# Optimization experiments

Hardware: AMD Instinct MI355X
Metric: run time of the kernel (lower is better)

Reference implementation:

```python
import jax, jax.numpy as jnp
import numpy as np

B, L, D = 4, 2048, 1024


def setup_inputs() -> dict:
    key = jax.random.key(0)
    ks = jax.random.split(key, 7)
    scale = 1.0 / np.sqrt(D)
    x = jax.random.normal(ks[0], (B, L, D), dtype=jnp.float32)
    wq = jax.random.normal(ks[1], (D, D), dtype=jnp.float32) * scale
    wk = jax.random.normal(ks[2], (D, D), dtype=jnp.float32) * scale
    wv = jax.random.normal(ks[3], (D, D), dtype=jnp.float32) * scale
    bq = jnp.zeros((D,), dtype=jnp.float32)
    bk = jnp.zeros((D,), dtype=jnp.float32)
    bv = jnp.zeros((D,), dtype=jnp.float32)
    # causal decoder mask, shape [B, 1, L, L] as produced by nn.make_causal_mask
    causal = jnp.tril(jnp.ones((L, L), dtype=bool))
    mask = jnp.broadcast_to(causal[None, None, :, :], (B, 1, L, L))
    return {"x": x, "mask": mask, "wq": wq, "bq": bq, "wk": wk, "bk": bk, "wv": wv, "bv": bv}


def reference(x, mask, wq, bq, wk, bk, wv, bv):
    # q/k/v projections (Dense with bias)
    q = x @ wq + bq            # [B, L, D]
    k = x @ wk + bk
    v = x @ wv + bv
    depth = q.shape[-1]
    q = q / jnp.sqrt(jnp.asarray(depth, dtype=q.dtype))
    attn = jnp.einsum('bqd,bkd->bqk', q, k)          # [B, L, L]
    attn = jnp.where(jnp.squeeze(mask), attn, -999999)
    attn = jax.nn.softmax(attn, axis=-1)
    out = attn @ v                                    # [B, L, D]
    return out
```

## Files before the change

### kernel.cpp

```cpp
#include <hip/hip_runtime.h>

typedef __bf16 bf16_t;
typedef __attribute__((ext_vector_type(8))) __bf16 bf16x8;
typedef __attribute__((ext_vector_type(4))) __bf16 bf16x4;
typedef __attribute__((ext_vector_type(4))) float f32x4;

#define B_  4
#define L_  2048
#define D_  1024
#define M_  (B_*L_)
#define N3_ (3*D_)

__device__ __forceinline__ void gload_lds16(const void* g, void* l) {
  __builtin_amdgcn_global_load_lds(
      (__attribute__((address_space(1))) void*)(g),
      (__attribute__((address_space(3))) void*)(l), 16, 0, 0);
}

__device__ __forceinline__ void stage_half(const bf16_t* __restrict__ g, int ld, int grow0,
                                           int k0, bf16_t* lds_tile, int h, int tid) {
  const int lane = tid & 63;
  const int csrc = ((lane & 7) ^ (lane >> 3)) << 3;
  const int rsub = tid >> 3;
  bf16_t* l0 = lds_tile + (size_t)(h * 128 + ((tid >> 6) << 3)) * 64;
  const bf16_t* g0 = g + (size_t)(grow0 + h * 128 + rsub) * ld + (k0 + csrc);
  gload_lds16(g0, l0);
  gload_lds16(g0 + (size_t)64 * ld, l0 + 64 * 64);
}

#define KTILE(J, AC, AN1, AN2, BCr, BNx, bC, bN)                                  \
  do {                                                                            \
    const int j_ = (J);                                                           \
    _Pragma("unroll")                                                             \
    for (int mi = 0; mi < 4; ++mi) {                                              \
      aM1_[mi][0] = *(const bf16x8*)(AC + abase + (4 + mi) * 2048 + co0);         \
      aM1_[mi][1] = *(const bf16x8*)(AC + abase + (4 + mi) * 2048 + co1);         \
    }                                                                             \
    if (j_ + 2 < NT) {                                                            \
      stage_half(A, lda, r0, (j_ + 2) * 64, AN2, 0, tid);                         \
      stage_half(A, lda, r0, (j_ + 2) * 64, AN2, 1, tid);                         \
    }                                                                             \
    asm volatile("s_waitcnt lgkmcnt(8)" ::: "memory");                            \
    __builtin_amdgcn_sched_barrier(0);                                            \
    __builtin_amdgcn_s_setprio(1);                                                \
    _Pragma("unroll")                                                             \
    for (int mi = 0; mi < 4; ++mi)                                                \
      _Pragma("unroll")                                                           \
      for (int ni = 0; ni < 2; ++ni) {                                            \
        acc[mi][ni] = __builtin_amdgcn_mfma_f32_16x16x32_bf16(                    \
            bC[ni][0], aM0_[mi][0], acc[mi][ni], 0, 0, 0);                        \
        acc[mi][ni] = __builtin_amdgcn_mfma_f32_16x16x32_bf16(                    \
            bC[ni][1], aM0_[mi][1], acc[mi][ni], 0, 0, 0);                        \
      }                                                                           \
    __builtin_amdgcn_s_setprio(0);                                                \
    if (j_ + 2 < NT) asm volatile("s_waitcnt vmcnt(4)" ::: "memory");             \
    else             asm volatile("s_waitcnt vmcnt(0)" ::: "memory");             \
    asm volatile("s_barrier" ::: "memory");                                       \
    if (j_ + 1 < NT) {                                                            \
      _Pragma("unroll")                                                           \
      for (int mi = 0; mi < 4; ++mi) {                                            \
        aM0_[mi][0] = *(const bf16x8*)(AN1 + abase + mi * 2048 + co0);            \
        aM0_[mi][1] = *(const bf16x8*)(AN1 + abase + mi * 2048 + co1);            \
      }                                                                           \
      _Pragma("unroll")                                                           \
      for (int ni = 0; ni < 2; ++ni) {                                            \
        bN[ni][0] = *(const bf16x8*)(BNx + bbase + ni * 1024 + co0);              \
        bN[ni][1] = *(const bf16x8*)(BNx + bbase + ni * 1024 + co1);              \
      }                                                                           \
      if (j_ + 2 < NT)                                                            \
        stage_half(Bt, ldb, c0, (j_ + 2) * 64, BCr, 0, tid);                      \
      asm volatile("s_waitcnt lgkmcnt(12)" ::: "memory");                         \
    } else {                                                                      \
      asm volatile("s_waitcnt lgkmcnt(0)" ::: "memory");                          \
    }                                                                             \
    __builtin_amdgcn_sched_barrier(0);                                            \
    __builtin_amdgcn_s_setprio(1);                                                \
    _Pragma("unroll")                                                             \
    for (int mi = 0; mi < 4; ++mi)                                                \
      _Pragma("unroll")                                                           \
      for (int ni = 0; ni < 2; ++ni) {                                            \
        acc[4 + mi][ni] = __builtin_amdgcn_mfma_f32_16x16x32_bf16(                \
            bC[ni][0], aM1_[mi][0], acc[4 + mi][ni], 0, 0, 0);                    \
        acc[4 + mi][ni] = __builtin_amdgcn_mfma_f32_16x16x32_bf16(                \
            bC[ni][1], aM1_[mi][1], acc[4 + mi][ni], 0, 0, 0);                    \
      }                                                                           \
    __builtin_amdgcn_s_setprio(0);                                                \
    asm volatile("s_barrier" ::: "memory");                                       \
  } while (0)

template<bool OUT_BF16, bool CAUSAL, bool VARK, bool PROJ>
__global__ __launch_bounds__(512, 2)
void gemm8(const bf16_t* __restrict__ A, int lda, long sA,
           const bf16_t* __restrict__ Bt, int ldb, long sB,
           void* __restrict__ Cv, int ldc, long sC,
           const float* __restrict__ b0, const float* __restrict__ b1,
           const float* __restrict__ b2, int K)
{
  const int gx = gridDim.x;
  const int nwg = gx * gridDim.y;
  const int orig = blockIdx.y * gx + blockIdx.x;
  const int swz = (orig & 7) * (nwg >> 3) + (orig >> 3);
  const int bx = swz % gx, by = swz / gx;
  if (CAUSAL && bx > 2 * by + 1) return;

  const int z = blockIdx.z;
  A  += (size_t)z * sA;
  Bt += (size_t)z * sB;

  const int r0 = by * 256, c0 = bx * 128;
  const int kend = VARK ? min(K, r0 + 256) : K;
  const int NT = kend >> 6;

  extern __shared__ __align__(16) bf16_t smem[];
  bf16_t* Ab0 = smem;
  bf16_t* Ab1 = smem + 16384;
  bf16_t* Ab2 = smem + 32768;
  bf16_t* Bb0 = smem + 49152;
  bf16_t* Bb1 = smem + 57344;

  const int tid = threadIdx.x;
  const int wid = tid >> 6, lane = tid & 63;
  const int wm = wid >> 2, wn = wid & 3;
  const int rl = lane & 15, cg = lane >> 4, x0 = lane & 7;
  const int co0 = ((cg ^ x0) << 3);
  const int co1 = (((4 + cg) ^ x0) << 3);
  const int abase = (wm * 16 + rl) * 64;
  const int bbase = (wn * 32 + rl) * 64;

  f32x4 acc[8][2] = {};
  bf16x8 aM0_[4][2], aM1_[4][2];
  bf16x8 bA_[2][2], bB_[2][2];

  stage_half(A,  lda, r0, 0,  Ab0, 0, tid);
  stage_half(A,  lda, r0, 0,  Ab0, 1, tid);
  stage_half(Bt, ldb, c0, 0,  Bb0, 0, tid);
  stage_half(A,  lda, r0, 64, Ab1, 0, tid);
  stage_half(A,  lda, r0, 64, Ab1, 1, tid);
  stage_half(Bt, ldb, c0, 64, Bb1, 0, tid);
  asm volatile("s_waitcnt vmcnt(6)" ::: "memory");
  asm volatile("s_barrier" ::: "memory");
  #pragma unroll
  for (int mi = 0; mi < 4; ++mi) {
    aM0_[mi][0] = *(const bf16x8*)(Ab0 + abase + mi * 2048 + co0);
    aM0_[mi][1] = *(const bf16x8*)(Ab0 + abase + mi * 2048 + co1);
  }
  #pragma unroll
  for (int ni = 0; ni < 2; ++ni) {
    bA_[ni][0] = *(const bf16x8*)(Bb0 + bbase + ni * 1024 + co0);
    bA_[ni][1] = *(const bf16x8*)(Bb0 + bbase + ni * 1024 + co1);
  }

  bf16_t *A0 = Ab0, *A1 = Ab1, *A2 = Ab2;
  for (int j = 0; j < NT; j += 2) {
    KTILE(j,     A0, A1, A2, Bb0, Bb1, bA_, bB_);
    KTILE(j + 1, A1, A2, A0, Bb1, Bb0, bB_, bA_);
    bf16_t* t = A2; A2 = A1; A1 = A0; A0 = t;
  }

  const int ml = lane & 15, ng = cg * 4;
  #pragma unroll
  for (int mi = 0; mi < 8; ++mi) {
    const int r = r0 + mi * 32 + wm * 16 + ml;
    #pragma unroll
    for (int ni = 0; ni < 2; ++ni) {
      const int c = c0 + wn * 32 + ni * 16 + ng;
      f32x4 v = acc[mi][ni];
      if (PROJ) {
        const float* bias = (c < D_) ? b0 : (c < 2 * D_) ? b1 : b2;
        const float4 bb = *(const float4*)(bias + (c & (D_ - 1)));
        const float sc = (c < D_) ? 0.03125f : 1.0f;
        v[0] = (v[0] + bb.x) * sc; v[1] = (v[1] + bb.y) * sc;
        v[2] = (v[2] + bb.z) * sc; v[3] = (v[3] + bb.w) * sc;
      }
      if (OUT_BF16) {
        bf16x4 o = {(bf16_t)v[0], (bf16_t)v[1], (bf16_t)v[2], (bf16_t)v[3]};
        *(bf16x4*)((bf16_t*)Cv + (size_t)z * sC + (size_t)r * ldc + c) = o;
      } else {
        *(f32x4*)((float*)Cv + (size_t)z * sC + (size_t)r * ldc + c) = v;
      }
    }
  }
}

__device__ __forceinline__ float blk_red_max(float v, float* red, int lane, int wid) {
  #pragma unroll
  for (int o = 32; o; o >>= 1) v = fmaxf(v, __shfl_down(v, o));
  __syncthreads();
  if (lane == 0) red[wid] = v;
  __syncthreads();
  return fmaxf(fmaxf(red[0], red[1]), fmaxf(red[2], red[3]));
}
__device__ __forceinline__ float blk_red_sum(float v, float* red, int lane, int wid) {
  #pragma unroll
  for (int o = 32; o; o >>= 1) v += __shfl_down(v, o);
  __syncthreads();
  if (lane == 0) red[wid] = v;
  __syncthreads();
  return red[0] + red[1] + red[2] + red[3];
}

__global__ __launch_bounds__(256)
void softmax_causal(const bf16_t* __restrict__ S, bf16_t* __restrict__ P) {
  const int r = blockIdx.x;
  const int n = r + 1;
  const int kend = min(((n + 255) >> 8) << 8, L_);
  const bf16_t* row = S + (size_t)blockIdx.y * L_ * L_ + (size_t)r * L_;
  bf16_t* prow = P + (size_t)blockIdx.y * L_ * L_ + (size_t)r * L_;
  const int tid = threadIdx.x, lane = tid & 63, wid = tid >> 6;
  const int c0 = tid * 8;
  __shared__ float red[4];

  const bf16x8 v8 = *(const bf16x8*)(row + c0);
  float s[8];
  #pragma unroll
  for (int i = 0; i < 8; ++i)
    s[i] = (c0 + i < n) ? (float)v8[i] : -3.402823466e38f;

  float mx = s[0];
  #pragma unroll
  for (int i = 1; i < 8; ++i) mx = fmaxf(mx, s[i]);
  mx = blk_red_max(mx, red, lane, wid);

  float e[8]; float sum = 0.f;
  #pragma unroll
  for (int i = 0; i < 8; ++i) {
    const float v = (c0 + i < n) ? __expf(s[i] - mx) : 0.f;
    e[i] = v; sum += v;
  }
  sum = blk_red_sum(sum, red, lane, wid);
  const float inv = 1.0f / sum;

  if (c0 < kend) {
    bf16x8 o;
    #pragma unroll
    for (int i = 0; i < 8; ++i) o[i] = (bf16_t)(e[i] * inv);
    *(bf16x8*)(prow + c0) = o;
  }
}

__global__ void cvt_f32_bf16(const float* __restrict__ in, bf16_t* __restrict__ out, int n4) {
  const int stride = gridDim.x * blockDim.x;
  for (int i = blockIdx.x * blockDim.x + threadIdx.x; i < n4; i += stride) {
    const float4 v = ((const float4*)in)[i];
    bf16x4 o = { (bf16_t)v.x, (bf16_t)v.y, (bf16_t)v.z, (bf16_t)v.w };
    ((bf16x4*)out)[i] = o;
  }
}

__global__ void transpose_w3(const float* __restrict__ w0, const float* __restrict__ w1,
                             const float* __restrict__ w2, bf16_t* __restrict__ oT) {
  const float* w = blockIdx.z == 0 ? w0 : (blockIdx.z == 1 ? w1 : w2);
  bf16_t* o = oT + (size_t)blockIdx.z * D_ * D_;
  __shared__ float t[32][33];
  const int tx = threadIdx.x, ty = threadIdx.y;
  const int x  = blockIdx.x * 32 + tx;
  const int y0 = blockIdx.y * 32;
  #pragma unroll
  for (int j = 0; j < 4; ++j)
    t[ty + j * 8][tx] = w[(size_t)(y0 + ty + j * 8) * D_ + x];
  __syncthreads();
  const int x2 = y0 + tx;
  const int y2 = blockIdx.x * 32;
  #pragma unroll
  for (int j = 0; j < 4; ++j)
    o[(size_t)(y2 + ty + j * 8) * D_ + x2] = (bf16_t)t[tx][ty + j * 8];
}

__global__ void transpose_bf16(const bf16_t* __restrict__ in, int ld_in, int coff,
                               bf16_t* __restrict__ out, int R, int C) {
  __shared__ bf16_t t[32][34];
  const int tx = threadIdx.x, ty = threadIdx.y;
  const int x  = blockIdx.x * 32 + tx;
  const int y0 = blockIdx.y * 32;
  #pragma unroll
  for (int j = 0; j < 4; ++j)
    t[ty + j * 8][tx] = in[(size_t)(y0 + ty + j * 8) * ld_in + coff + x];
  __syncthreads();
  const int x2 = y0 + tx;
  const int y2 = blockIdx.x * 32;
  #pragma unroll
  for (int j = 0; j < 4; ++j)
    out[(size_t)(y2 + ty + j * 8) * R + x2] = t[tx][ty + j * 8];
}

extern "C" void kernel_launch(void* const* d_in, const int* in_sizes, int n_in,
                              void* d_out, int out_size, void* d_ws, size_t ws_size,
                              hipStream_t stream) {
  const float* x  = (const float*)d_in[0];
  const float* wq = (const float*)d_in[2];
  const float* bq = (const float*)d_in[3];
  const float* wk = (const float*)d_in[4];
  const float* bk = (const float*)d_in[5];
  const float* wv = (const float*)d_in[6];
  const float* bv = (const float*)d_in[7];
  float* out = (float*)d_out;

  bf16_t* xb   = (bf16_t*)d_ws;
  bf16_t* wT   = xb  + (size_t)M_ * D_;
  bf16_t* qkv  = wT  + (size_t)N3_ * D_;
  bf16_t* vbT  = qkv + (size_t)M_ * N3_;
  bf16_t* Sb   = vbT + (size_t)M_ * D_;
  bf16_t* Pfull = qkv;

  const size_t SMEM = 131072;

  cvt_f32_bf16<<<1024, 256, 0, stream>>>(x, xb, M_ * D_ / 4);
  transpose_w3<<<dim3(32, 32, 3), dim3(32, 8), 0, stream>>>(wq, wk, wv, wT);

  gemm8<true, false, false, true><<<dim3(N3_ / 128, M_ / 256), 512, SMEM, stream>>>(
      xb, D_, 0, wT, D_, 0, qkv, N3_, 0, bq, bk, bv, D_);

  transpose_bf16<<<dim3(D_ / 32, M_ / 32), dim3(32, 8), 0, stream>>>(qkv, N3_, 2 * D_, vbT, M_, D_);

  gemm8<true, true, false, false><<<dim3(L_ / 128, L_ / 256, B_), 512, SMEM, stream>>>(
      qkv, N3_, (long)L_ * N3_, qkv + D_, N3_, (long)L_ * N3_, Sb, L_, (long)L_ * L_,
      nullptr, nullptr, nullptr, D_);

  softmax_causal<<<dim3(L_, B_), 256, 0, stream>>>(Sb, Pfull);

  gemm8<false, false, true, false><<<dim3(D_ / 128, L_ / 256, B_), 512, SMEM, stream>>>(
      Pfull, L_, (long)L_ * L_, vbT, M_, (long)L_, out, D_, (long)L_ * D_,
      nullptr, nullptr, nullptr, L_);
}
```

Before: 179.2 us.

## Load-balance causal PV GEMM with split-K band jobs and partial-sum reduction

Replaces the uniform PV GEMM launch with a job kernel that assigns causal row bands to workgroups in balanced pairs. The longest bands are split along K, with one part written to a float workspace and then added back by a small reduction kernel. The aim is to remove the load imbalance caused by the triangular attention matrix, at the cost of an extra kernel launch and a read-modify-write of part of the output.

```diff
diff --git a/kernel.cpp b/kernel.cpp
--- a/kernel.cpp
+++ b/kernel.cpp
@@ -182,6 +182,116 @@
   }
 }
 
+__global__ __launch_bounds__(512, 2)
+void pv_job(const bf16_t* __restrict__ A_, int lda, long sA,
+            const bf16_t* __restrict__ Bt_, int ldb, long sB,
+            float* __restrict__ out, int ldc, long sC,
+            float* __restrict__ part)
+{
+  const int gx = gridDim.x;
+  const int nwg = gx * gridDim.y;
+  const int orig = blockIdx.y * gx + blockIdx.x;
+  const int swz = (orig & 7) * (nwg >> 3) + (orig >> 3);
+  const int bx = swz % gx, yy = swz / gx;
+
+  const int z = blockIdx.z;
+  const bf16_t* A  = A_  + (size_t)z * sA;
+  const bf16_t* Bt = Bt_ + (size_t)z * sB;
+  const int c0 = bx * 128;
+
+  int nseg = 1, band0, j00 = 0, nt0, band1 = 0, j01 = 0, nt1 = 0;
+  bool topart = false;
+  switch (yy) {
+    case 0:  band0 = 3; nt0 = 16; break;
+    case 1:  band0 = 4; nt0 = 20; break;
+    case 2:  nseg = 2; band0 = 0; nt0 = 4;  band1 = 7; j01 = 0; nt1 = 14; break;
+    case 3:  band0 = 7; j00 = 14; nt0 = 32; topart = true; break;
+    case 4:  nseg = 2; band0 = 1; nt0 = 8;  band1 = 6; j01 = 0; nt1 = 10; break;
+    case 5:  band0 = 6; j00 = 10; nt0 = 28; topart = true; break;
+    case 6:  nseg = 2; band0 = 2; nt0 = 12; band1 = 5; j01 = 0; nt1 = 6; break;
+    default: band0 = 5; j00 = 6;  nt0 = 24; topart = true; break;
+  }
+
+  extern __shared__ __align__(16) bf16_t smem[];
+  bf16_t* Ab0 = smem;
+  bf16_t* Ab1 = smem + 16384;
+  bf16_t* Ab2 = smem + 32768;
+  bf16_t* Bb0 = smem + 49152;
+  bf16_t* Bb1 = smem + 57344;
+
+  const int tid = threadIdx.x;
+  const int wid = tid >> 6, lane = tid & 63;
+  const int wm = wid >> 2, wn = wid & 3;
+  const int rl = lane & 15, cg = lane >> 4, x0 = lane & 7;
+  const int co0 = ((cg ^ x0) << 3);
+  const int co1 = (((4 + cg) ^ x0) << 3);
+  const int abase = (wm * 16 + rl) * 64;
+  const int bbase = (wn * 32 + rl) * 64;
+
+  for (int seg = 0; seg < nseg; ++seg) {
+    const int r0 = (seg ? band1 : band0) * 256;
+    const int j0 = seg ? j01 : j00;
+    const int NT = seg ? nt1 : nt0;
+    const bool pw = (seg == 0) && topart;
+
+    f32x4 acc[8][2] = {};
+    bf16x8 aM0_[4][2], aM1_[4][2];
+    bf16x8 bA_[2][2], bB_[2][2];
+
+    stage_half(A,  lda, r0, j0 * 64,       Ab0, 0, tid);
+    stage_half(A,  lda, r0, j0 * 64,       Ab0, 1, tid);
+    stage_half(Bt, ldb, c0, j0 * 64,       Bb0, 0, tid);
+    stage_half(A,  lda, r0, (j0 + 1) * 64, Ab1, 0, tid);
+    stage_half(A,  lda, r0, (j0 + 1) * 64, Ab1, 1, tid);
+    stage_half(Bt, ldb, c0, (j0 + 1) * 64, Bb1, 0, tid);
+    asm volatile("s_waitcnt vmcnt(6)" ::: "memory");
+    asm volatile("s_barrier" ::: "memory");
+    #pragma unroll
+    for (int mi = 0; mi < 4; ++mi) {
+      aM0_[mi][0] = *(const bf16x8*)(Ab0 + abase + mi * 2048 + co0);
+      aM0_[mi][1] = *(const bf16x8*)(Ab0 + abase + mi * 2048 + co1);
+    }
+    #pragma unroll
+    for (int ni = 0; ni < 2; ++ni) {
+      bA_[ni][0] = *(const bf16x8*)(Bb0 + bbase + ni * 1024 + co0);
+      bA_[ni][1] = *(const bf16x8*)(Bb0 + bbase + ni * 1024 + co1);
+    }
+
+    bf16_t *A0 = Ab0, *A1 = Ab1, *A2 = Ab2;
+    for (int j = j0; j < NT; j += 2) {
+      KTILE(j,     A0, A1, A2, Bb0, Bb1, bA_, bB_);
+      KTILE(j + 1, A1, A2, A0, Bb1, Bb0, bB_, bA_);
+      bf16_t* t = A2; A2 = A1; A1 = A0; A0 = t;
+    }
+
+    const int ml = lane & 15, ng = cg * 4;
+    #pragma unroll
+    for (int mi = 0; mi < 8; ++mi) {
+      const int r = r0 + mi * 32 + wm * 16 + ml;
+      #pragma unroll
+      for (int ni = 0; ni < 2; ++ni) {
+        const int c = c0 + wn * 32 + ni * 16 + ng;
+        float* dst = pw
+            ? part + (size_t)z * (768 * 1024) + (size_t)(r - 1280) * 1024 + c
+            : out + (size_t)z * sC + (size_t)r * ldc + c;
+        *(f32x4*)dst = acc[mi][ni];
+      }
+    }
+    if (seg + 1 < nseg) __syncthreads();
+  }
+}
+
+__global__ void add_partial(float* __restrict__ out, const float* __restrict__ part) {
+  const int i = blockIdx.x * blockDim.x + threadIdx.x;
+  const int z = i / 196608;
+  const int o = i - z * 196608;
+  float4* dst = (float4*)(out + (size_t)z * L_ * D_ + 1280 * D_) + o;
+  const float4 p = ((const float4*)(part + (size_t)z * 768 * 1024))[o];
+  float4 d = *dst;
+  d.x += p.x; d.y += p.y; d.z += p.z; d.w += p.w;
+  *dst = d;
+}
+
 __device__ __forceinline__ float blk_red_max(float v, float* red, int lane, int wid) {
   #pragma unroll
   for (int o = 32; o; o >>= 1) v = fmaxf(v, __shfl_down(v, o));
@@ -301,6 +411,7 @@
   bf16_t* vbT  = qkv + (size_t)M_ * N3_;
   bf16_t* Sb   = vbT + (size_t)M_ * D_;
   bf16_t* Pfull = qkv;
+  float*  part = (float*)Sb;
 
   const size_t SMEM = 131072;
 
@@ -318,7 +429,8 @@
 
   softmax_causal<<<dim3(L_, B_), 256, 0, stream>>>(Sb, Pfull);
 
-  gemm8<false, false, true, false><<<dim3(D_ / 128, L_ / 256, B_), 512, SMEM, stream>>>(
-      Pfull, L_, (long)L_ * L_, vbT, M_, (long)L_, out, D_, (long)L_ * D_,
-      nullptr, nullptr, nullptr, L_);
-}
+  pv_job<<<dim3(8, 8, B_), 512, SMEM, stream>>>(
+      Pfull, L_, (long)L_ * L_, vbT, M_, (long)L_, out, D_, (long)L_ * D_, part);
+
+  add_partial<<<3072, 256, 0, stream>>>(out, part);
+}
```

Result: no change. 180.7 us (+0.9%).

## Use 256x256-tile four-phase ping-pong kernel for the QKV projection GEMM

Applied to the files above, without the earlier changes.

Replaces the 256x128-tile gemm8 instance for the fused QKV projection with a dedicated kernel that computes 256x256 output tiles. Each k-step is split into four MFMA quadrant phases, with A and B loads interleaved between them and double-buffered in LDS. This aims to raise arithmetic intensity and cut global and LDS traffic per FLOP. The costs are more accumulator registers (32 f32x4 per thread), more barriers per k-step, and half as many workgroups, which lowers parallelism.

```diff
diff --git a/kernel.cpp b/kernel.cpp
--- a/kernel.cpp
+++ b/kernel.cpp
@@ -26,6 +26,150 @@
   const bf16_t* g0 = g + (size_t)(grow0 + h * 128 + rsub) * ld + (k0 + csrc);
   gload_lds16(g0, l0);
   gload_lds16(g0 + (size_t)64 * ld, l0 + 64 * 64);
+}
+
+#define MFMA_BF16 __builtin_amdgcn_mfma_f32_16x16x32_bf16
+
+__global__ __launch_bounds__(512, 2)
+void proj8ph(const bf16_t* __restrict__ A, int lda,
+             const bf16_t* __restrict__ Bt, int ldb,
+             bf16_t* __restrict__ C, int ldc,
+             const float* __restrict__ b0, const float* __restrict__ b1,
+             const float* __restrict__ b2, int K)
+{
+  const int gx = gridDim.x;
+  const int nwg = gx * gridDim.y;
+  const int orig = blockIdx.y * gx + blockIdx.x;
+  const int swz = (orig & 7) * (nwg >> 3) + (orig >> 3);
+  const int bx = swz % gx, by = swz / gx;
+  const int r0 = by * 256, c0 = bx * 256;
+  const int NT = K >> 6;
+
+  extern __shared__ __align__(16) bf16_t smem[];
+
+  const int tid = threadIdx.x;
+  const int wid = tid >> 6, lane = tid & 63;
+  const int wm = wid >> 2, wn = wid & 3;
+  const int rl = lane & 15, cg = lane >> 4, x0 = lane & 7;
+  const int co0 = ((cg ^ x0) << 3);
+  const int co1 = (((4 + cg) ^ x0) << 3);
+  const int abase = (wm * 128 + rl) * 64;
+  const int bbase = (wn * 64 + rl) * 64;
+
+  f32x4 acc[8][4] = {};
+  bf16x8 aLo[4][2], aHi[4][2], bLo[2][2], bHi[2][2];
+
+  stage_half(A,  lda, r0, 0,  smem,         0, tid);
+  stage_half(A,  lda, r0, 0,  smem,         1, tid);
+  stage_half(Bt, ldb, c0, 0,  smem + 32768, 0, tid);
+  stage_half(Bt, ldb, c0, 0,  smem + 32768, 1, tid);
+  stage_half(A,  lda, r0, 64, smem + 16384, 0, tid);
+  stage_half(A,  lda, r0, 64, smem + 16384, 1, tid);
+  asm volatile("s_waitcnt vmcnt(0)" ::: "memory");
+  asm volatile("s_barrier" ::: "memory");
+
+  for (int t = 0; t < NT; ++t) {
+    bf16_t* Ab = smem + (t & 1) * 16384;
+    bf16_t* Bb = smem + 32768 + (t & 1) * 16384;
+    bf16_t* Bn = smem + 32768 + ((t + 1) & 1) * 16384;
+
+    #pragma unroll
+    for (int mi = 0; mi < 4; ++mi) {
+      aLo[mi][0] = *(const bf16x8*)(Ab + abase + mi * 1024 + co0);
+      aLo[mi][1] = *(const bf16x8*)(Ab + abase + mi * 1024 + co1);
+    }
+    #pragma unroll
+    for (int ni = 0; ni < 2; ++ni) {
+      bLo[ni][0] = *(const bf16x8*)(Bb + bbase + ni * 1024 + co0);
+      bLo[ni][1] = *(const bf16x8*)(Bb + bbase + ni * 1024 + co1);
+    }
+    if (t + 1 < NT) stage_half(Bt, ldb, c0, (t + 1) * 64, Bn, 0, tid);
+    asm volatile("s_waitcnt lgkmcnt(8)" ::: "memory");
+    asm volatile("s_barrier" ::: "memory");
+    asm volatile("s_waitcnt lgkmcnt(0)" ::: "memory");
+    __builtin_amdgcn_sched_barrier(0);
+    __builtin_amdgcn_s_setprio(1);
+    #pragma unroll
+    for (int mi = 0; mi < 4; ++mi)
+      #pragma unroll
+      for (int ni = 0; ni < 2; ++ni) {
+        acc[mi][ni] = MFMA_BF16(bLo[ni][0], aLo[mi][0], acc[mi][ni], 0, 0, 0);
+        acc[mi][ni] = MFMA_BF16(bLo[ni][1], aLo[mi][1], acc[mi][ni], 0, 0, 0);
+      }
+    __builtin_amdgcn_s_setprio(0);
+    asm volatile("s_barrier" ::: "memory");
+
+    #pragma unroll
+    for (int mi = 0; mi < 4; ++mi) {
+      aHi[mi][0] = *(const bf16x8*)(Ab + abase + (4 + mi) * 1024 + co0);
+      aHi[mi][1] = *(const bf16x8*)(Ab + abase + (4 + mi) * 1024 + co1);
+    }
+    if (t + 1 < NT) stage_half(Bt, ldb, c0, (t + 1) * 64, Bn, 1, tid);
+    asm volatile("s_barrier" ::: "memory");
+    asm volatile("s_waitcnt lgkmcnt(0)" ::: "memory");
+    __builtin_amdgcn_sched_barrier(0);
+    __builtin_amdgcn_s_setprio(1);
+    #pragma unroll
+    for (int mi = 0; mi < 4; ++mi)
+      #pragma unroll
+      for (int ni = 0; ni < 2; ++ni) {
+        acc[4 + mi][ni] = MFMA_BF16(bLo[ni][0], aHi[mi][0], acc[4 + mi][ni], 0, 0, 0);
+        acc[4 + mi][ni] = MFMA_BF16(bLo[ni][1], aHi[mi][1], acc[4 + mi][ni], 0, 0, 0);
+      }
+    __builtin_amdgcn_s_setprio(0);
+    asm volatile("s_barrier" ::: "memory");
+
+    #pragma unroll
+    for (int ni = 0; ni < 2; ++ni) {
+      bHi[ni][0] = *(const bf16x8*)(Bb + bbase + (2 + ni) * 1024 + co0);
+      bHi[ni][1] = *(const bf16x8*)(Bb + bbase + (2 + ni) * 1024 + co1);
+    }
+    if (t + 2 < NT) stage_half(A, lda, r0, (t + 2) * 64, Ab, 0, tid);
+    asm volatile("s_barrier" ::: "memory");
+    asm volatile("s_waitcnt lgkmcnt(0)" ::: "memory");
+    __builtin_amdgcn_sched_barrier(0);
+    __builtin_amdgcn_s_setprio(1);
+    #pragma unroll
+    for (int mi = 0; mi < 4; ++mi)
+      #pragma unroll
+      for (int ni = 0; ni < 2; ++ni) {
+        acc[mi][2 + ni] = MFMA_BF16(bHi[ni][0], aLo[mi][0], acc[mi][2 + ni], 0, 0, 0);
+        acc[mi][2 + ni] = MFMA_BF16(bHi[ni][1], aLo[mi][1], acc[mi][2 + ni], 0, 0, 0);
+      }
+    __builtin_amdgcn_s_setprio(0);
+    asm volatile("s_barrier" ::: "memory");
+
+    if (t + 2 < NT) stage_half(A, lda, r0, (t + 2) * 64, Ab, 1, tid);
+    __builtin_amdgcn_s_setprio(1);
+    #pragma unroll
+    for (int mi = 0; mi < 4; ++mi)
+      #pragma unroll
+      for (int ni = 0; ni < 2; ++ni) {
+        acc[4 + mi][2 + ni] = MFMA_BF16(bHi[ni][0], aHi[mi][0], acc[4 + mi][2 + ni], 0, 0, 0);
+        acc[4 + mi][2 + ni] = MFMA_BF16(bHi[ni][1], aHi[mi][1], acc[4 + mi][2 + ni], 0, 0, 0);
+      }
+    __builtin_amdgcn_s_setprio(0);
+    if (t + 2 < NT) asm volatile("s_waitcnt vmcnt(4)" ::: "memory");
+    else            asm volatile("s_waitcnt vmcnt(0)" ::: "memory");
+    asm volatile("s_barrier" ::: "memory");
+  }
+
+  const int ng = cg * 4;
+  #pragma unroll
+  for (int mi = 0; mi < 8; ++mi) {
+    const int r = r0 + wm * 128 + mi * 16 + rl;
+    #pragma unroll
+    for (int ni = 0; ni < 4; ++ni) {
+      const int c = c0 + wn * 64 + ni * 16 + ng;
+      const float* bias = (c < D_) ? b0 : (c < 2 * D_) ? b1 : b2;
+      const float4 bb = *(const float4*)(bias + (c & (D_ - 1)));
+      const float sc = (c < D_) ? 0.03125f : 1.0f;
+      f32x4 v = acc[mi][ni];
+      bf16x4 o = {(bf16_t)((v[0] + bb.x) * sc), (bf16_t)((v[1] + bb.y) * sc),
+                  (bf16_t)((v[2] + bb.z) * sc), (bf16_t)((v[3] + bb.w) * sc)};
+      *(bf16x4*)(C + (size_t)r * ldc + c) = o;
+    }
+  }
 }
 
 #define KTILE(J, AC, AN1, AN2, BCr, BNx, bC, bN)                                  \
@@ -47,10 +191,8 @@
     for (int mi = 0; mi < 4; ++mi)                                                \
       _Pragma("unroll")                                                           \
       for (int ni = 0; ni < 2; ++ni) {                                            \
-        acc[mi][ni] = __builtin_amdgcn_mfma_f32_16x16x32_bf16(                    \
-            bC[ni][0], aM0_[mi][0], acc[mi][ni], 0, 0, 0);                        \
-        acc[mi][ni] = __builtin_amdgcn_mfma_f32_16x16x32_bf16(                    \
-            bC[ni][1], aM0_[mi][1], acc[mi][ni], 0, 0, 0);                        \
+        acc[mi][ni] = MFMA_BF16(bC[ni][0], aM0_[mi][0], acc[mi][ni], 0, 0, 0);    \
+        acc[mi][ni] = MFMA_BF16(bC[ni][1], aM0_[mi][1], acc[mi][ni], 0, 0, 0);    \
       }                                                                           \
     __builtin_amdgcn_s_setprio(0);                                                \
     if (j_ + 2 < NT) asm volatile("s_waitcnt vmcnt(4)" ::: "memory");             \
@@ -79,22 +221,18 @@
     for (int mi = 0; mi < 4; ++mi)                                                \
       _Pragma("unroll")                                                           \
       for (int ni = 0; ni < 2; ++ni) {                                            \
-        acc[4 + mi][ni] = __builtin_amdgcn_mfma_f32_16x16x32_bf16(                \
-            bC[ni][0], aM1_[mi][0], acc[4 + mi][ni], 0, 0, 0);                    \
-        acc[4 + mi][ni] = __builtin_amdgcn_mfma_f32_16x16x32_bf16(                \
-            bC[ni][1], aM1_[mi][1], acc[4 + mi][ni], 0, 0, 0);                    \
+        acc[4 + mi][ni] = MFMA_BF16(bC[ni][0], aM1_[mi][0], acc[4 + mi][ni], 0, 0, 0); \
+        acc[4 + mi][ni] = MFMA_BF16(bC[ni][1], aM1_[mi][1], acc[4 + mi][ni], 0, 0, 0); \
       }                                                                           \
     __builtin_amdgcn_s_setprio(0);                                                \
     asm volatile("s_barrier" ::: "memory");                                       \
   } while (0)
 
-template<bool OUT_BF16, bool CAUSAL, bool VARK, bool PROJ>
+template<bool OUT_BF16, bool CAUSAL, bool VARK>
 __global__ __launch_bounds__(512, 2)
 void gemm8(const bf16_t* __restrict__ A, int lda, long sA,
            const bf16_t* __restrict__ Bt, int ldb, long sB,
-           void* __restrict__ Cv, int ldc, long sC,
-           const float* __restrict__ b0, const float* __restrict__ b1,
-           const float* __restrict__ b2, int K)
+           void* __restrict__ Cv, int ldc, long sC, int K)
 {
   const int gx = gridDim.x;
   const int nwg = gx * gridDim.y;
@@ -165,13 +303,6 @@
     for (int ni = 0; ni < 2; ++ni) {
       const int c = c0 + wn * 32 + ni * 16 + ng;
       f32x4 v = acc[mi][ni];
-      if (PROJ) {
-        const float* bias = (c < D_) ? b0 : (c < 2 * D_) ? b1 : b2;
-        const float4 bb = *(const float4*)(bias + (c & (D_ - 1)));
-        const float sc = (c < D_) ? 0.03125f : 1.0f;
-        v[0] = (v[0] + bb.x) * sc; v[1] = (v[1] + bb.y) * sc;
-        v[2] = (v[2] + bb.z) * sc; v[3] = (v[3] + bb.w) * sc;
-      }
       if (OUT_BF16) {
         bf16x4 o = {(bf16_t)v[0], (bf16_t)v[1], (bf16_t)v[2], (bf16_t)v[3]};
         *(bf16x4*)((bf16_t*)Cv + (size_t)z * sC + (size_t)r * ldc + c) = o;
@@ -307,18 +438,16 @@
   cvt_f32_bf16<<<1024, 256, 0, stream>>>(x, xb, M_ * D_ / 4);
   transpose_w3<<<dim3(32, 32, 3), dim3(32, 8), 0, stream>>>(wq, wk, wv, wT);
 
-  gemm8<true, false, false, true><<<dim3(N3_ / 128, M_ / 256), 512, SMEM, stream>>>(
-      xb, D_, 0, wT, D_, 0, qkv, N3_, 0, bq, bk, bv, D_);
+  proj8ph<<<dim3(N3_ / 256, M_ / 256), 512, SMEM, stream>>>(
+      xb, D_, wT, D_, qkv, N3_, bq, bk, bv, D_);
 
   transpose_bf16<<<dim3(D_ / 32, M_ / 32), dim3(32, 8), 0, stream>>>(qkv, N3_, 2 * D_, vbT, M_, D_);
 
-  gemm8<true, true, false, false><<<dim3(L_ / 128, L_ / 256, B_), 512, SMEM, stream>>>(
-      qkv, N3_, (long)L_ * N3_, qkv + D_, N3_, (long)L_ * N3_, Sb, L_, (long)L_ * L_,
-      nullptr, nullptr, nullptr, D_);
+  gemm8<true, true, false><<<dim3(L_ / 128, L_ / 256, B_), 512, SMEM, stream>>>(
+      qkv, N3_, (long)L_ * N3_, qkv + D_, N3_, (long)L_ * N3_, Sb, L_, (long)L_ * L_, D_);
 
   softmax_causal<<<dim3(L_, B_), 256, 0, stream>>>(Sb, Pfull);
 
-  gemm8<false, false, true, false><<<dim3(D_ / 128, L_ / 256, B_), 512, SMEM, stream>>>(
-      Pfull, L_, (long)L_ * L_, vbT, M_, (long)L_, out, D_, (long)L_ * D_,
-      nullptr, nullptr, nullptr, L_);
-}
+  gemm8<false, false, true><<<dim3(D_ / 128, L_ / 256, B_), 512, SMEM, stream>>>(
+      Pfull, L_, (long)L_ * L_, vbT, M_, (long)L_, out, D_, (long)L_ * D_, L_);
+}
```

Result: slower. 188.9 us (+5.4%).

## Switch GEMMs to 128x128 tiles with 4-wave 2x2 warp layout

Applied to the files above, without the earlier changes.

Replaces the 256x128 tile, 8-wave GEMM with a 128x128 tile, 4-wave kernel where each wave computes a 64x64 sub-block (2x4 fragments per half). LDS staging, wait counts, causal tile-skip condition, VARK k-range and shared memory size are all adjusted to the smaller tile. The intent is finer-grained causal skipping and variable-K trimming plus more workgroups for load balance, at the cost of lower per-tile arithmetic intensity and more global traffic per FLOP.

```diff
diff --git a/kernel.cpp b/kernel.cpp
--- a/kernel.cpp
+++ b/kernel.cpp
@@ -17,36 +17,35 @@
       (__attribute__((address_space(3))) void*)(l), 16, 0, 0);
 }
 
-__device__ __forceinline__ void stage_half(const bf16_t* __restrict__ g, int ld, int grow0,
-                                           int k0, bf16_t* lds_tile, int h, int tid) {
+__device__ __forceinline__ void stage_tile4(const bf16_t* __restrict__ g, int ld, int grow0,
+                                            int k0, bf16_t* lds_tile, int tid) {
   const int lane = tid & 63;
   const int csrc = ((lane & 7) ^ (lane >> 3)) << 3;
   const int rsub = tid >> 3;
-  bf16_t* l0 = lds_tile + (size_t)(h * 128 + ((tid >> 6) << 3)) * 64;
-  const bf16_t* g0 = g + (size_t)(grow0 + h * 128 + rsub) * ld + (k0 + csrc);
+  bf16_t* l0 = lds_tile + (size_t)((tid >> 6) << 3) * 64;
+  const bf16_t* g0 = g + (size_t)(grow0 + rsub) * ld + (k0 + csrc);
   gload_lds16(g0, l0);
+  gload_lds16(g0 + (size_t)32 * ld, l0 + 32 * 64);
   gload_lds16(g0 + (size_t)64 * ld, l0 + 64 * 64);
-}
-
-#define KTILE(J, AC, AN1, AN2, BCr, BNx, bC, bN)                                  \
+  gload_lds16(g0 + (size_t)96 * ld, l0 + 96 * 64);
+}
+
+#define KTILE4(J, AC, AN1, AN2, BCr, BNx, bC, bN)                                 \
   do {                                                                            \
     const int j_ = (J);                                                           \
     _Pragma("unroll")                                                             \
-    for (int mi = 0; mi < 4; ++mi) {                                              \
-      aM1_[mi][0] = *(const bf16x8*)(AC + abase + (4 + mi) * 2048 + co0);         \
-      aM1_[mi][1] = *(const bf16x8*)(AC + abase + (4 + mi) * 2048 + co1);         \
+    for (int mi = 0; mi < 2; ++mi) {                                              \
+      aM1_[mi][0] = *(const bf16x8*)(AC + abase + (2 + mi) * 1024 + co0);         \
+      aM1_[mi][1] = *(const bf16x8*)(AC + abase + (2 + mi) * 1024 + co1);         \
     }                                                                             \
-    if (j_ + 2 < NT) {                                                            \
-      stage_half(A, lda, r0, (j_ + 2) * 64, AN2, 0, tid);                         \
-      stage_half(A, lda, r0, (j_ + 2) * 64, AN2, 1, tid);                         \
-    }                                                                             \
-    asm volatile("s_waitcnt lgkmcnt(8)" ::: "memory");                            \
+    if (j_ + 2 < NT) stage_tile4(A, lda, r0, (j_ + 2) * 64, AN2, tid);            \
+    asm volatile("s_waitcnt lgkmcnt(4)" ::: "memory");                            \
     __builtin_amdgcn_sched_barrier(0);                                            \
     __builtin_amdgcn_s_setprio(1);                                                \
     _Pragma("unroll")                                                             \
-    for (int mi = 0; mi < 4; ++mi)                                                \
+    for (int mi = 0; mi < 2; ++mi)                                                \
       _Pragma("unroll")                                                           \
-      for (int ni = 0; ni < 2; ++ni) {                                            \
+      for (int ni = 0; ni < 4; ++ni) {                                            \
         acc[mi][ni] = __builtin_amdgcn_mfma_f32_16x16x32_bf16(                    \
             bC[ni][0], aM0_[mi][0], acc[mi][ni], 0, 0, 0);                        \
         acc[mi][ni] = __builtin_amdgcn_mfma_f32_16x16x32_bf16(                    \
@@ -58,17 +57,16 @@
     asm volatile("s_barrier" ::: "memory");                                       \
     if (j_ + 1 < NT) {                                                            \
       _Pragma("unroll")                                                           \
-      for (int mi = 0; mi < 4; ++mi) {                                            \
-        aM0_[mi][0] = *(const bf16x8*)(AN1 + abase + mi * 2048 + co0);            \
-        aM0_[mi][1] = *(const bf16x8*)(AN1 + abase + mi * 2048 + co1);            \
+      for (int mi = 0; mi < 2; ++mi) {                                            \
+        aM0_[mi][0] = *(const bf16x8*)(AN1 + abase + mi * 1024 + co0);            \
+        aM0_[mi][1] = *(const bf16x8*)(AN1 + abase + mi * 1024 + co1);            \
       }                                                                           \
       _Pragma("unroll")                                                           \
-      for (int ni = 0; ni < 2; ++ni) {                                            \
+      for (int ni = 0; ni < 4; ++ni) {                                            \
         bN[ni][0] = *(const bf16x8*)(BNx + bbase + ni * 1024 + co0);              \
         bN[ni][1] = *(const bf16x8*)(BNx + bbase + ni * 1024 + co1);              \
       }                                                                           \
-      if (j_ + 2 < NT)                                                            \
-        stage_half(Bt, ldb, c0, (j_ + 2) * 64, BCr, 0, tid);                      \
+      if (j_ + 2 < NT) stage_tile4(Bt, ldb, c0, (j_ + 2) * 64, BCr, tid);         \
       asm volatile("s_waitcnt lgkmcnt(12)" ::: "memory");                         \
     } else {                                                                      \
       asm volatile("s_waitcnt lgkmcnt(0)" ::: "memory");                          \
@@ -76,21 +74,21 @@
     __builtin_amdgcn_sched_barrier(0);                                            \
     __builtin_amdgcn_s_setprio(1);                                                \
     _Pragma("unroll")                                                             \
-    for (int mi = 0; mi < 4; ++mi)                                                \
+    for (int mi = 0; mi < 2; ++mi)                                                \
       _Pragma("unroll")                                                           \
-      for (int ni = 0; ni < 2; ++ni) {                                            \
-        acc[4 + mi][ni] = __builtin_amdgcn_mfma_f32_16x16x32_bf16(                \
-            bC[ni][0], aM1_[mi][0], acc[4 + mi][ni], 0, 0, 0);                    \
-        acc[4 + mi][ni] = __builtin_amdgcn_mfma_f32_16x16x32_bf16(                \
-            bC[ni][1], aM1_[mi][1], acc[4 + mi][ni], 0, 0, 0);                    \
+      for (int ni = 0; ni < 4; ++ni) {                                            \
+        acc[2 + mi][ni] = __builtin_amdgcn_mfma_f32_16x16x32_bf16(                \
+            bC[ni][0], aM1_[mi][0], acc[2 + mi][ni], 0, 0, 0);                    \
+        acc[2 + mi][ni] = __builtin_amdgcn_mfma_f32_16x16x32_bf16(                \
+            bC[ni][1], aM1_[mi][1], acc[2 + mi][ni], 0, 0, 0);                    \
       }                                                                           \
     __builtin_amdgcn_s_setprio(0);                                                \
     asm volatile("s_barrier" ::: "memory");                                       \
   } while (0)
 
 template<bool OUT_BF16, bool CAUSAL, bool VARK, bool PROJ>
-__global__ __launch_bounds__(512, 2)
-void gemm8(const bf16_t* __restrict__ A, int lda, long sA,
+__global__ __launch_bounds__(256, 2)
+void gemm4(const bf16_t* __restrict__ A, int lda, long sA,
            const bf16_t* __restrict__ Bt, int ldb, long sB,
            void* __restrict__ Cv, int ldc, long sC,
            const float* __restrict__ b0, const float* __restrict__ b1,
@@ -101,69 +99,67 @@
   const int orig = blockIdx.y * gx + blockIdx.x;
   const int swz = (orig & 7) * (nwg >> 3) + (orig >> 3);
   const int bx = swz % gx, by = swz / gx;
-  if (CAUSAL && bx > 2 * by + 1) return;
+  if (CAUSAL && bx > by) return;
 
   const int z = blockIdx.z;
   A  += (size_t)z * sA;
   Bt += (size_t)z * sB;
 
-  const int r0 = by * 256, c0 = bx * 128;
-  const int kend = VARK ? min(K, r0 + 256) : K;
+  const int r0 = by * 128, c0 = bx * 128;
+  const int kend = VARK ? min(K, r0 + 128) : K;
   const int NT = kend >> 6;
 
   extern __shared__ __align__(16) bf16_t smem[];
   bf16_t* Ab0 = smem;
-  bf16_t* Ab1 = smem + 16384;
-  bf16_t* Ab2 = smem + 32768;
-  bf16_t* Bb0 = smem + 49152;
-  bf16_t* Bb1 = smem + 57344;
+  bf16_t* Ab1 = smem + 8192;
+  bf16_t* Ab2 = smem + 16384;
+  bf16_t* Bb0 = smem + 24576;
+  bf16_t* Bb1 = smem + 32768;
 
   const int tid = threadIdx.x;
   const int wid = tid >> 6, lane = tid & 63;
-  const int wm = wid >> 2, wn = wid & 3;
+  const int wm = wid >> 1, wn = wid & 1;
   const int rl = lane & 15, cg = lane >> 4, x0 = lane & 7;
   const int co0 = ((cg ^ x0) << 3);
   const int co1 = (((4 + cg) ^ x0) << 3);
-  const int abase = (wm * 16 + rl) * 64;
-  const int bbase = (wn * 32 + rl) * 64;
-
-  f32x4 acc[8][2] = {};
-  bf16x8 aM0_[4][2], aM1_[4][2];
-  bf16x8 bA_[2][2], bB_[2][2];
-
-  stage_half(A,  lda, r0, 0,  Ab0, 0, tid);
-  stage_half(A,  lda, r0, 0,  Ab0, 1, tid);
-  stage_half(Bt, ldb, c0, 0,  Bb0, 0, tid);
-  stage_half(A,  lda, r0, 64, Ab1, 0, tid);
-  stage_half(A,  lda, r0, 64, Ab1, 1, tid);
-  stage_half(Bt, ldb, c0, 64, Bb1, 0, tid);
-  asm volatile("s_waitcnt vmcnt(6)" ::: "memory");
+  const int abase = (wm * 64 + rl) * 64;
+  const int bbase = (wn * 64 + rl) * 64;
+
+  f32x4 acc[4][4] = {};
+  bf16x8 aM0_[2][2], aM1_[2][2];
+  bf16x8 bA_[4][2], bB_[4][2];
+
+  stage_tile4(A,  lda, r0, 0,  Ab0, tid);
+  stage_tile4(Bt, ldb, c0, 0,  Bb0, tid);
+  stage_tile4(A,  lda, r0, 64, Ab1, tid);
+  stage_tile4(Bt, ldb, c0, 64, Bb1, tid);
+  asm volatile("s_waitcnt vmcnt(8)" ::: "memory");
   asm volatile("s_barrier" ::: "memory");
   #pragma unroll
-  for (int mi = 0; mi < 4; ++mi) {
-    aM0_[mi][0] = *(const bf16x8*)(Ab0 + abase + mi * 2048 + co0);
-    aM0_[mi][1] = *(const bf16x8*)(Ab0 + abase + mi * 2048 + co1);
-  }
-  #pragma unroll
-  for (int ni = 0; ni < 2; ++ni) {
+  for (int mi = 0; mi < 2; ++mi) {
+    aM0_[mi][0] = *(const bf16x8*)(Ab0 + abase + mi * 1024 + co0);
+    aM0_[mi][1] = *(const bf16x8*)(Ab0 + abase + mi * 1024 + co1);
+  }
+  #pragma unroll
+  for (int ni = 0; ni < 4; ++ni) {
     bA_[ni][0] = *(const bf16x8*)(Bb0 + bbase + ni * 1024 + co0);
     bA_[ni][1] = *(const bf16x8*)(Bb0 + bbase + ni * 1024 + co1);
   }
 
   bf16_t *A0 = Ab0, *A1 = Ab1, *A2 = Ab2;
   for (int j = 0; j < NT; j += 2) {
-    KTILE(j,     A0, A1, A2, Bb0, Bb1, bA_, bB_);
-    KTILE(j + 1, A1, A2, A0, Bb1, Bb0, bB_, bA_);
+    KTILE4(j,     A0, A1, A2, Bb0, Bb1, bA_, bB_);
+    KTILE4(j + 1, A1, A2, A0, Bb1, Bb0, bB_, bA_);
     bf16_t* t = A2; A2 = A1; A1 = A0; A0 = t;
   }
 
   const int ml = lane & 15, ng = cg * 4;
   #pragma unroll
-  for (int mi = 0; mi < 8; ++mi) {
-    const int r = r0 + mi * 32 + wm * 16 + ml;
+  for (int mi = 0; mi < 4; ++mi) {
+    const int r = r0 + wm * 64 + mi * 16 + ml;
     #pragma unroll
-    for (int ni = 0; ni < 2; ++ni) {
-      const int c = c0 + wn * 32 + ni * 16 + ng;
+    for (int ni = 0; ni < 4; ++ni) {
+      const int c = c0 + wn * 64 + ni * 16 + ng;
       f32x4 v = acc[mi][ni];
       if (PROJ) {
         const float* bias = (c < D_) ? b0 : (c < 2 * D_) ? b1 : b2;
@@ -302,23 +298,23 @@
   bf16_t* Sb   = vbT + (size_t)M_ * D_;
   bf16_t* Pfull = qkv;
 
-  const size_t SMEM = 131072;
+  const size_t SMEM = 81920;
 
   cvt_f32_bf16<<<1024, 256, 0, stream>>>(x, xb, M_ * D_ / 4);
   transpose_w3<<<dim3(32, 32, 3), dim3(32, 8), 0, stream>>>(wq, wk, wv, wT);
 
-  gemm8<true, false, false, true><<<dim3(N3_ / 128, M_ / 256), 512, SMEM, stream>>>(
+  gemm4<true, false, false, true><<<dim3(N3_ / 128, M_ / 128), 256, SMEM, stream>>>(
       xb, D_, 0, wT, D_, 0, qkv, N3_, 0, bq, bk, bv, D_);
 
   transpose_bf16<<<dim3(D_ / 32, M_ / 32), dim3(32, 8), 0, stream>>>(qkv, N3_, 2 * D_, vbT, M_, D_);
 
-  gemm8<true, true, false, false><<<dim3(L_ / 128, L_ / 256, B_), 512, SMEM, stream>>>(
+  gemm4<true, true, false, false><<<dim3(L_ / 128, L_ / 128, B_), 256, SMEM, stream>>>(
       qkv, N3_, (long)L_ * N3_, qkv + D_, N3_, (long)L_ * N3_, Sb, L_, (long)L_ * L_,
       nullptr, nullptr, nullptr, D_);
 
   softmax_causal<<<dim3(L_, B_), 256, 0, stream>>>(Sb, Pfull);
 
-  gemm8<false, false, true, false><<<dim3(D_ / 128, L_ / 256, B_), 512, SMEM, stream>>>(
+  gemm4<false, false, true, false><<<dim3(D_ / 128, L_ / 128, B_), 256, SMEM, stream>>>(
       Pfull, L_, (long)L_ * L_, vbT, M_, (long)L_, out, D_, (long)L_ * D_,
       nullptr, nullptr, nullptr, L_);
 }
```

Measured after the change: 168.3 us, median of 3. 6.0% less time.
